# Kernel tuning notes

Measured on AMD Instinct MI355X. Metric: run time of the kernel, lower is better.

The kernel has to match this reference:

```python
import jax, jax.numpy as jnp
import numpy as np


def _layernorm(x, g, b, eps=1e-5):
    m = x.mean(-1, keepdims=True)
    v = ((x - m) ** 2).mean(-1, keepdims=True)
    return (x - m) * jax.lax.rsqrt(v + eps) * g + b


def _rmsnorm(x, w, eps=1e-6):
    return x * jax.lax.rsqrt((x * x).mean(-1, keepdims=True) + eps) * w


def setup_inputs() -> dict:
    key = jax.random.key(0)
    ks = jax.random.split(key, 8)
    B, T, S, C_img = 1, 3, 880, 3072
    C_mouse, D_hid, Dd = 2, 1024, 64
    vin = C_img + 12 * C_mouse  # 3096 = img_hidden + mouse_dim_in*vae_tcr*windows
    w = lambda k, shp: (jax.random.normal(k, shp, jnp.float32) * 0.02)
    return dict(
        x=jax.random.normal(ks[0], (B, T * S, C_img), jnp.float32),
        condition=jax.random.normal(ks[1], (B, 12, C_mouse), jnp.float32),
        w1=w(ks[2], (vin, D_hid)), b1=jnp.zeros((D_hid,), jnp.float32),
        w2=w(ks[3], (D_hid, D_hid)), b2=jnp.zeros((D_hid,), jnp.float32),
        ln_g=jnp.ones((D_hid,), jnp.float32), ln_b=jnp.zeros((D_hid,), jnp.float32),
        wqkv=w(ks[4], (D_hid, 3 * D_hid)), bqkv=jnp.zeros((3 * D_hid,), jnp.float32),
        qn_w=jnp.ones((Dd,), jnp.float32), kn_w=jnp.ones((Dd,), jnp.float32),
        wproj=w(ks[5], (D_hid, C_img)), bproj=jnp.zeros((C_img,), jnp.float32),
        H=22, W=40, temporal_shape=3, num_frame_per_block=3,
    )


def reference(x, condition, w1, b1, w2, b2, ln_g, ln_b, wqkv, bqkv,
              qn_w, kn_w, wproj, bproj, H, W, temporal_shape, num_frame_per_block):
    B, T_S, C_img = x.shape
    T = temporal_shape
    if condition.shape[1] > 9:
        condition = condition[:, -12:, :]
    _, N_frames, C = condition.shape
    action_len, pad_len = 20, 12
    pad = jnp.zeros((B, action_len - N_frames, C), condition.dtype)
    mouse_padded = jnp.concatenate([pad, condition], axis=1)  # [B, 20, C]
    # windowed gather: fixed small loop over num_frame_per_block (<=3)
    wins = jnp.stack([mouse_padded[:, i * 4:i * 4 + pad_len, :]
                      for i in range(num_frame_per_block)], axis=1)  # [B, F, 12, C]
    gm = wins.reshape(B, num_frame_per_block, pad_len * C)  # [B, F, 12C]
    S = 880  # hardcoded in original forward
    gm = jnp.broadcast_to(gm[:, None], (B, S, num_frame_per_block, pad_len * C))
    gm = gm.reshape(B * S, num_frame_per_block, pad_len * C)
    # fuse broadcast mouse features with image tokens (raw row-major reshape, as in torch)
    fused = jnp.concatenate([x.reshape(B * S, T, C_img), gm], axis=-1)  # [BS, T, C_img+12C]
    h = jax.nn.gelu(fused @ w1 + b1, approximate=True) @ w2 + b2
    h = _layernorm(h, ln_g, ln_b)  # [BS, T, D_hid]
    qkv = h @ wqkv + bqkv  # [BS, T, 3*D_hid]
    Dd = qn_w.shape[0]
    Hh = qkv.shape[-1] // (3 * Dd)
    qkv = qkv.reshape(B * S, T, 3, Hh, Dd)
    q, k, v = qkv[:, :, 0], qkv[:, :, 1], qkv[:, :, 2]
    q = _rmsnorm(q, qn_w).astype(v.dtype)
    k = _rmsnorm(k, kn_w).astype(v.dtype)
    # original flattens to one sequence of BS*T tokens for single_prefill (non-causal)
    N = B * S * T
    qf = q.reshape(N, Hh, Dd)
    kf = k.reshape(N, Hh, Dd)
    vf = v.reshape(N, Hh, Dd)
    scale = 1.0 / np.sqrt(Dd).astype(np.float32)
    scores = jnp.einsum('nhd,mhd->hnm', qf, kf) * scale  # [Hh, N, N]
    attn = jax.nn.softmax(scores, axis=-1)
    o = jnp.einsum('hnm,mhd->nhd', attn, vf)  # [N, Hh, Dd]
    # '(B S) T H D -> B (T S) (H D)'
    o = o.reshape(B, S, T, Hh, Dd).transpose(0, 2, 1, 3, 4).reshape(B, T * S, Hh * Dd)
    out = o @ wproj + bproj
    return x + out
```

## Files before the change

kernel.cpp:

```cpp
#include <hip/hip_runtime.h>
#include <hip/hip_bf16.h>

typedef __attribute__((ext_vector_type(8))) short short8;
typedef __attribute__((ext_vector_type(4))) short short4v;
typedef __attribute__((ext_vector_type(4))) unsigned uint4v;
typedef __attribute__((ext_vector_type(4))) float f32x4;
typedef __attribute__((ext_vector_type(16))) float f32x16;
typedef unsigned short u16;

#define ZERO16 (f32x16){0,0,0,0,0,0,0,0,0,0,0,0,0,0,0,0}

__device__ __forceinline__ float b2f(u16 h) {
    unsigned u = ((unsigned)h) << 16;
    float f; __builtin_memcpy(&f, &u, 4); return f;
}
__device__ __forceinline__ u16 f2b(float f) {
    __hip_bfloat16 h = __float2bfloat16(f);
    u16 r; __builtin_memcpy(&r, &h, 2); return r;
}
__device__ __forceinline__ void gload16(const void* g, void* l) {
    __builtin_amdgcn_global_load_lds(
        (const __attribute__((address_space(1))) unsigned*)g,
        (__attribute__((address_space(3))) unsigned*)l, 16, 0, 0);
}
__device__ __forceinline__ unsigned cvtpk_bf16(float lo, float hi) {
    unsigned d;
    asm("v_cvt_pk_bf16_f32 %0, %1, %2" : "=v"(d) : "v"(lo), "v"(hi));
    return d;
}

#define M_VALID 2640
#define M_PAD   2688
#define K1P     3072
#define DH      1024
#define CIMG    3072
#define NHEAD   16
#define NT      84
#define QTP     42
#define NSPLIT  3
#define TILES_PER_SPLIT 28
#define LOG2E   1.4426950408889634f

__global__ __launch_bounds__(256) void build_fused_kernel(
    const float* __restrict__ x, u16* __restrict__ fused)
{
    int n = blockIdx.x;
    int tid = threadIdx.x;
    const float* xr = x + (size_t)n * CIMG;
    u16* fr = fused + (size_t)n * K1P;
    for (int c = tid * 4; c < CIMG; c += 1024) {
        float4 v = *(const float4*)(xr + c);
        short4v w;
        w[0] = (short)f2b(v.x); w[1] = (short)f2b(v.y);
        w[2] = (short)f2b(v.z); w[3] = (short)f2b(v.w);
        *(short4v*)(fr + c) = w;
    }
}

__global__ __launch_bounds__(256) void bias1t_kernel(
    const float* __restrict__ w1, const float* __restrict__ b1,
    const float* __restrict__ cond, float* __restrict__ bias1t)
{
    int t = blockIdx.x;
    int col = blockIdx.y * 256 + threadIdx.x;
    float v = b1[col];
#pragma unroll
    for (int j = 0; j < 24; j++) {
        int f = t * 4 + (j >> 1);
        if (f >= 8) v += cond[(f - 8) * 2 + (j & 1)] * w1[(size_t)(3072 + j) * DH + col];
    }
    bias1t[t * DH + col] = v;
}

__global__ __launch_bounds__(256) void transpose_all_kernel(
    const float* __restrict__ w1, const float* __restrict__ w2,
    const float* __restrict__ wqkv, const float* __restrict__ wproj,
    u16* __restrict__ w1t, u16* __restrict__ w2t,
    u16* __restrict__ wqkvt, u16* __restrict__ wprojt)
{
    int b = blockIdx.x;
    const float* W; u16* Wt; int K, N, ldt, nx;
    if (b < 3072)      {            W = w1;    Wt = w1t;    K = 3072; N = DH;   ldt = 3072; nx = 32; }
    else if (b < 4096) { b -= 3072; W = w2;    Wt = w2t;    K = DH;   N = DH;   ldt = DH;   nx = 32; }
    else if (b < 7168) { b -= 4096; W = wqkv;  Wt = wqkvt;  K = DH;   N = 3072; ldt = DH;   nx = 96; }
    else               { b -= 7168; W = wproj; Wt = wprojt; K = DH;   N = CIMG; ldt = DH;   nx = 96; }
    __shared__ float t[32][33];
    int n0 = (b % nx) * 32, k0 = (b / nx) * 32;
    int x = threadIdx.x & 31, y0 = threadIdx.x >> 5;
    for (int yy = y0; yy < 32; yy += 8) {
        int k = k0 + yy, n = n0 + x;
        t[yy][x] = (k < K && n < N) ? W[(size_t)k * N + n] : 0.f;
    }
    __syncthreads();
    for (int yy = y0; yy < 32; yy += 8) {
        int n = n0 + yy, k = k0 + x;
        if (n < N && k < ldt) Wt[(size_t)n * ldt + k] = f2b(t[x][yy]);
    }
}

template<int EPI, int BM, int BN>
__global__ __launch_bounds__(256) void gemm_kernel(
    const u16* __restrict__ A, const u16* __restrict__ Bt,
    const float* __restrict__ bias, const float* __restrict__ resid,
    u16* __restrict__ Cb, float* __restrict__ Cf,
    int N, int K, int Mvalid)
{
    constexpr int MI  = BM / 32;
    constexpr int NJ  = BN / 32;
    constexpr int CA  = BM / 32;
    constexpr int CB  = BN / 32;
    constexpr unsigned ABYTES = BM * 128;
    constexpr unsigned BBYTES = BN * 128;
    constexpr unsigned STG = 2 * (ABYTES + BBYTES);
    constexpr unsigned CTW = BN + 4;
    constexpr unsigned CTB = BM * CTW * 4;
    constexpr int TPR = 256 / BM;
    __shared__ __align__(16) char smem[STG > CTB ? STG : CTB];

    const int tid = threadIdx.x;
    const int lane = tid & 63, wid = tid >> 6;
    const int l15 = lane & 15, l4 = lane >> 4;

    const int nx = N / BN;
    const int nwg = nx * (M_PAD / BM);
    const int bid = blockIdx.x;
    const int wgid = (bid & 7) * (nwg >> 3) + (bid >> 3);
    const int m0 = (wgid / nx) * BM, n0 = (wgid % nx) * BN;

    const int wr = (wid >> 1) * (BM / 2), wc = (wid & 1) * (BN / 2);

    const int srow = lane >> 3;
    const int scol = ((lane & 7) ^ (lane >> 3)) << 3;

    f32x4 acc[MI][NJ];
#pragma unroll
    for (int i = 0; i < MI; i++)
#pragma unroll
        for (int j = 0; j < NJ; j++) acc[i][j] = (f32x4){0.f, 0.f, 0.f, 0.f};

    const int nt = K >> 6;

    auto stage = [&](int buf, int k0) {
        char* Ab = smem + buf * ABYTES;
        char* Bb = smem + 2 * ABYTES + buf * BBYTES;
#pragma unroll
        for (int i = 0; i < CA; i++) {
            int c = wid * CA + i;
            gload16(A + (size_t)(m0 + c * 8 + srow) * K + k0 + scol,
                    Ab + c * 1024 + lane * 16);
        }
#pragma unroll
        for (int i = 0; i < CB; i++) {
            int c = wid * CB + i;
            gload16(Bt + (size_t)(n0 + c * 8 + srow) * K + k0 + scol,
                    Bb + c * 1024 + lane * 16);
        }
    };

    stage(0, 0);
    __syncthreads();
    int cur = 0;
    for (int t = 0; t < nt; t++) {
        if (t + 1 < nt) stage(cur ^ 1, (t + 1) * 64);
        const char* Ab = smem + cur * ABYTES;
        const char* Bb = smem + 2 * ABYTES + cur * BBYTES;
#pragma unroll
        for (int ki = 0; ki < 2; ki++) {
            short8 af[MI], bfr[NJ];
#pragma unroll
            for (int i = 0; i < MI; i++) {
                int row = wr + i * 16 + l15;
                af[i] = *(const short8*)(Ab + row * 128 + (((ki * 4 + l4) ^ (l15 & 7)) << 4));
            }
#pragma unroll
            for (int j = 0; j < NJ; j++) {
                int row = wc + j * 16 + l15;
                bfr[j] = *(const short8*)(Bb + row * 128 + (((ki * 4 + l4) ^ (l15 & 7)) << 4));
            }
            __builtin_amdgcn_s_setprio(1);
#pragma unroll
            for (int i = 0; i < MI; i++)
#pragma unroll
                for (int j = 0; j < NJ; j++)
                    acc[i][j] = __builtin_amdgcn_mfma_f32_16x16x32_bf16(af[i], bfr[j], acc[i][j], 0, 0, 0);
            __builtin_amdgcn_s_setprio(0);
        }
        __syncthreads();
        cur ^= 1;
    }

    float* Ct = (float*)smem;
#pragma unroll
    for (int i = 0; i < MI; i++)
#pragma unroll
        for (int j = 0; j < NJ; j++)
#pragma unroll
            for (int r = 0; r < 4; r++)
                Ct[(wr + i * 16 + l4 * 4 + r) * CTW + wc + j * 16 + l15] = acc[i][j][r];
    __syncthreads();

    const int row = tid / TPR;
    const int cb  = (tid % TPR) * (BN / TPR);
    const int grow = m0 + row;
    const int gcol = n0 + cb;
    if (EPI == 2) {
        if (grow < Mvalid) {
#pragma unroll
            for (int u = 0; u < BN / (4 * TPR); u++) {
                f32x4 v = *(const f32x4*)&Ct[row * CTW + cb + u * 4];
                float4 bv = *(const float4*)&bias[gcol + u * 4];
                float4 rv = *(const float4*)&resid[(size_t)grow * N + gcol + u * 4];
                float4 o;
                o.x = v[0] + bv.x + rv.x; o.y = v[1] + bv.y + rv.y;
                o.z = v[2] + bv.z + rv.z; o.w = v[3] + bv.w + rv.w;
                *(float4*)&Cf[(size_t)grow * N + gcol + u * 4] = o;
            }
        }
    } else {
        const float* bb = bias + (EPI == 0 ? (size_t)(grow % 3) * N : 0);
        u16 tmp[BN / TPR];
#pragma unroll
        for (int u = 0; u < BN / (4 * TPR); u++) {
            f32x4 v = *(const f32x4*)&Ct[row * CTW + cb + u * 4];
            float4 bv = *(const float4*)&bb[gcol + u * 4];
#pragma unroll
            for (int e = 0; e < 4; e++) {
                float val = v[e] + ((const float*)&bv)[e];
                if (EPI == 0) {
                    float tt = val + 0.044715f * val * val * val;
                    val = 0.5f * val * (1.0f + tanhf(0.7978845608028654f * tt));
                }
                tmp[u * 4 + e] = f2b(val);
            }
        }
#pragma unroll
        for (int u = 0; u < BN / (8 * TPR); u++)
            *(short8*)(Cb + (size_t)grow * N + gcol + u * 8) = *(const short8*)&tmp[u * 8];
    }
}

__global__ __launch_bounds__(256) void ln_kernel(
    const u16* __restrict__ h2, const float* __restrict__ g,
    const float* __restrict__ b, u16* __restrict__ out)
{
    int row = blockIdx.x;
    int tid = threadIdx.x;
    const u16* p = h2 + (size_t)row * DH;
    float v[4];
#pragma unroll
    for (int i = 0; i < 4; i++) v[i] = b2f(p[tid * 4 + i]);
    float s1 = v[0] + v[1] + v[2] + v[3];
    float s2 = v[0]*v[0] + v[1]*v[1] + v[2]*v[2] + v[3]*v[3];
    for (int m = 1; m < 64; m <<= 1) { s1 += __shfl_xor(s1, m); s2 += __shfl_xor(s2, m); }
    __shared__ float a1[4], a2[4];
    int w = tid >> 6;
    if ((tid & 63) == 0) { a1[w] = s1; a2[w] = s2; }
    __syncthreads();
    s1 = a1[0] + a1[1] + a1[2] + a1[3];
    s2 = a2[0] + a2[1] + a2[2] + a2[3];
    float mean = s1 * (1.0f / 1024.0f);
    float var = s2 * (1.0f / 1024.0f) - mean * mean;
    float rs = rsqrtf(var + 1e-5f);
    u16* q = out + (size_t)row * DH;
#pragma unroll
    for (int i = 0; i < 4; i++) {
        int c = tid * 4 + i;
        q[c] = f2b((v[i] - mean) * rs * g[c] + b[c]);
    }
}

__global__ __launch_bounds__(256) void fragmentize_kernel(
    const u16* __restrict__ qkv, const float* __restrict__ qw, const float* __restrict__ kw,
    u16* __restrict__ Qf, u16* __restrict__ Kf, u16* __restrict__ Vf)
{
    __shared__ u16 Vlds[8 * 32 * 80];
    const int kt = blockIdx.x;
    const int hg = blockIdx.y;
    const int tid = threadIdx.x;
    const int t32 = tid >> 3, c8 = tid & 7;
    const int n = kt * 32 + t32;
    const u16* row = qkv + (size_t)n * 3072;

#pragma unroll
    for (int hh = 0; hh < 8; hh++) {
        short8 v = *(const short8*)(row + 2048 + (hg * 8 + hh) * 64 + c8 * 8);
        *(short8*)(&Vlds[(hh * 32 + t32) * 80 + c8 * 8]) = v;
    }

    float sq[8], sk[8];
#pragma unroll
    for (int hh = 0; hh < 8; hh++) {
        int h = hg * 8 + hh;
        short8 qv = *(const short8*)(row + h * 64 + c8 * 8);
        short8 kv = *(const short8*)(row + 1024 + h * 64 + c8 * 8);
        float aq = 0.f, ak = 0.f;
#pragma unroll
        for (int e = 0; e < 8; e++) {
            float fq = b2f((u16)qv[e]); aq += fq * fq;
            float fk = b2f((u16)kv[e]); ak += fk * fk;
        }
        sq[hh] = aq; sk[hh] = ak;
    }
#pragma unroll
    for (int m = 1; m < 8; m <<= 1) {
#pragma unroll
        for (int hh = 0; hh < 8; hh++) {
            sq[hh] += __shfl_xor(sq[hh], m);
            sk[hh] += __shfl_xor(sk[hh], m);
        }
    }

    float qwv[8], kwv[8];
#pragma unroll
    for (int e = 0; e < 8; e++) { qwv[e] = qw[c8 * 8 + e]; kwv[e] = kw[c8 * 8 + e]; }

#pragma unroll
    for (int hh = 0; hh < 8; hh++) {
        int h = hg * 8 + hh;
        float rq = rsqrtf(sq[hh] * (1.0f / 64.0f) + 1e-6f) * (0.125f * LOG2E);
        float rk = rsqrtf(sk[hh] * (1.0f / 64.0f) + 1e-6f);
        short8 qv = *(const short8*)(row + h * 64 + c8 * 8);
        short8 kv = *(const short8*)(row + 1024 + h * 64 + c8 * 8);
        short8 qo, ko;
#pragma unroll
        for (int e = 0; e < 8; e++) {
            qo[e] = (short)f2b(b2f((u16)qv[e]) * rq * qwv[e]);
            ko[e] = (short)f2b(b2f((u16)kv[e]) * rk * kwv[e]);
        }
        size_t base = (((size_t)(h * NT + kt) * 4 + (c8 >> 1)) << 9) + t32 * 16 + (c8 & 1) * 8;
        *(short8*)(Qf + base) = qo;
        *(short8*)(Kf + base) = ko;
    }

    __syncthreads();

    const int fd = tid >> 6;
    const int lkq = (tid & 63) >> 1, lhi = tid & 1;
#pragma unroll
    for (int hh = 0; hh < 8; hh++) {
        int h = hg * 8 + hh;
        short8 o;
#pragma unroll
        for (int e = 0; e < 8; e++)
            o[e] = (short)Vlds[(hh * 32 + (fd & 1) * 16 + lhi * 8 + e) * 80 + (fd >> 1) * 32 + lkq];
        *(short8*)(Vf + (((size_t)(h * NT + kt) * 4 + fd) << 9) + lkq * 16 + lhi * 8) = o;
    }
}

__device__ __forceinline__ void attn_tile(
    f32x16& st, float& lr, f32x16& o0, f32x16& o1,
    const u16* __restrict__ Vh, int tile, int lxy)
{
    short8 vv[4];
#pragma unroll
    for (int fd = 0; fd < 4; fd++)
        vv[fd] = *(const short8*)(Vh + (((size_t)tile * 4 + fd) << 9) + lxy);

    float p[16];
#pragma unroll
    for (int r = 0; r < 16; r++) p[r] = __builtin_amdgcn_exp2f(st[r]);
    float s0 = (p[0] + p[1]) + (p[2] + p[3]);
    float s1 = (p[4] + p[5]) + (p[6] + p[7]);
    float s2 = (p[8] + p[9]) + (p[10] + p[11]);
    float s3 = (p[12] + p[13]) + (p[14] + p[15]);
    float sum = (s0 + s1) + (s2 + s3);
    lr += sum + __shfl_xor(sum, 32);

    unsigned a0 = cvtpk_bf16(p[0], p[1]),   a1 = cvtpk_bf16(p[2], p[3]);
    unsigned a2 = cvtpk_bf16(p[4], p[5]),   a3 = cvtpk_bf16(p[6], p[7]);
    unsigned a4 = cvtpk_bf16(p[8], p[9]),   a5 = cvtpk_bf16(p[10], p[11]);
    unsigned a6 = cvtpk_bf16(p[12], p[13]), a7 = cvtpk_bf16(p[14], p[15]);
    asm("v_permlane32_swap_b32 %0, %1" : "+v"(a0), "+v"(a2));
    asm("v_permlane32_swap_b32 %0, %1" : "+v"(a1), "+v"(a3));
    asm("v_permlane32_swap_b32 %0, %1" : "+v"(a4), "+v"(a6));
    asm("v_permlane32_swap_b32 %0, %1" : "+v"(a5), "+v"(a7));
    uint4v u0 = {a0, a1, a2, a3}, u1 = {a4, a5, a6, a7};
    short8 pa0, pa1;
    __builtin_memcpy(&pa0, &u0, 16);
    __builtin_memcpy(&pa1, &u1, 16);

    __builtin_amdgcn_s_setprio(1);
    o0 = __builtin_amdgcn_mfma_f32_32x32x16_bf16(pa0, vv[0], o0, 0, 0, 0);
    o0 = __builtin_amdgcn_mfma_f32_32x32x16_bf16(pa1, vv[1], o0, 0, 0, 0);
    o1 = __builtin_amdgcn_mfma_f32_32x32x16_bf16(pa0, vv[2], o1, 0, 0, 0);
    o1 = __builtin_amdgcn_mfma_f32_32x32x16_bf16(pa1, vv[3], o1, 0, 0, 0);
    __builtin_amdgcn_s_setprio(0);
}

__global__ __launch_bounds__(128, 2) void attn_kernel(
    const u16* __restrict__ Qf, const u16* __restrict__ Kf,
    const u16* __restrict__ Vf, u16* __restrict__ part, float* __restrict__ ml)
{
    const int nwg = NSPLIT * NHEAD * QTP;
    const int bid = blockIdx.x;
    const int wgid = (bid & 7) * (nwg >> 3) + (bid >> 3);
    const int s   = wgid / (NHEAD * QTP);
    const int rem = wgid % (NHEAD * QTP);
    const int h   = rem / QTP;
    const int qtp = rem % QTP;
    const int wid = threadIdx.x >> 6;
    const int qt  = qtp * 2 + wid;
    const int lane = threadIdx.x & 63;
    const int kq = lane & 31;
    const int hi = lane >> 5;
    const int q0 = qt * 32;
    const int lxy = kq * 16 + hi * 8;
    const u16* Kh = Kf + ((size_t)h * NT * 4 << 9);
    const u16* Vh = Vf + ((size_t)h * NT * 4 << 9);

    short8 qf[4];
#pragma unroll
    for (int d = 0; d < 4; d++)
        qf[d] = *(const short8*)(Qf + (((size_t)(h * NT + qt) * 4 + d) << 9) + lxy);

    f32x16 o0 = ZERO16, o1 = ZERO16;
    float lr = 0.f;
    const int ts0 = s * TILES_PER_SPLIT;

    auto loadK = [&](short8* k, int tile) {
#pragma unroll
        for (int d = 0; d < 4; d++)
            k[d] = *(const short8*)(Kh + (((size_t)tile * 4 + d) << 9) + lxy);
    };
    auto qk = [&](const short8* k) {
        f32x16 st = ZERO16;
        __builtin_amdgcn_s_setprio(1);
#pragma unroll
        for (int d = 0; d < 4; d++)
            st = __builtin_amdgcn_mfma_f32_32x32x16_bf16(k[d], qf[d], st, 0, 0, 0);
        __builtin_amdgcn_s_setprio(0);
        return st;
    };
    auto mask = [&](f32x16& st, int tile) {
        const int k0 = tile * 32;
        if (k0 + 32 > M_VALID) {
#pragma unroll
            for (int r = 0; r < 16; r++) {
                int key = k0 + (r & 3) + 8 * (r >> 2) + 4 * hi;
                if (key >= M_VALID) st[r] = -3.0e38f;
            }
        }
    };

    short8 kfA[4], kfB[4];
    loadK(kfA, ts0);
    loadK(kfB, ts0 + 1);

    for (int i = 0; i < TILES_PER_SPLIT; i += 2) {
        const int t0 = ts0 + i, t1 = t0 + 1;
        f32x16 st0 = qk(kfA);
        f32x16 st1 = qk(kfB);
        if (i + 2 < TILES_PER_SPLIT) { loadK(kfA, t0 + 2); loadK(kfB, t0 + 3); }
        mask(st0, t0);
        attn_tile(st0, lr, o0, o1, Vh, t0, lxy);
        mask(st1, t1);
        attn_tile(st1, lr, o0, o1, Vh, t1, lxy);
    }

#pragma unroll
    for (int r = 0; r < 16; r++) {
        int rl = (r & 3) + 8 * (r >> 2) + 4 * hi;
        int qrow = q0 + rl;
        if (qrow < M_VALID) {
            u16* pp = part + ((size_t)s * M_PAD + qrow) * DH + h * 64;
            pp[kq] = f2b(o0[r]);
            pp[kq + 32] = f2b(o1[r]);
        }
    }
    if (hi == 0 && q0 + kq < M_VALID)
        ml[((size_t)s * NHEAD + h) * M_PAD + q0 + kq] = lr;
}

__global__ __launch_bounds__(256) void attn_merge_kernel(
    const u16* __restrict__ part, const float* __restrict__ ml, u16* __restrict__ obf)
{
    const int q = blockIdx.x;
    const int t = threadIdx.x;
    const int h = t >> 4, i = t & 15;
    float L = 0.f;
#pragma unroll
    for (int s = 0; s < NSPLIT; s++)
        L += ml[((size_t)s * NHEAD + h) * M_PAD + q];
    float inv = 1.0f / L;
    float4 acc = {0.f, 0.f, 0.f, 0.f};
#pragma unroll
    for (int s = 0; s < NSPLIT; s++) {
        short4v v = *(const short4v*)(part + ((size_t)s * M_PAD + q) * DH + h * 64 + i * 4);
        acc.x += b2f((u16)v[0]); acc.y += b2f((u16)v[1]);
        acc.z += b2f((u16)v[2]); acc.w += b2f((u16)v[3]);
    }
    int mrow = (q % 3) * 880 + q / 3;
    short4v w;
    w[0] = (short)f2b(acc.x * inv); w[1] = (short)f2b(acc.y * inv);
    w[2] = (short)f2b(acc.z * inv); w[3] = (short)f2b(acc.w * inv);
    *(short4v*)(obf + (size_t)mrow * DH + h * 64 + i * 4) = w;
}

extern "C" void kernel_launch(void* const* d_in, const int* in_sizes, int n_in,
                              void* d_out, int out_size, void* d_ws, size_t ws_size,
                              hipStream_t stream)
{
    const float* x      = (const float*)d_in[0];
    const float* cond   = (const float*)d_in[1];
    const float* w1     = (const float*)d_in[2];
    const float* b1     = (const float*)d_in[3];
    const float* w2     = (const float*)d_in[4];
    const float* b2     = (const float*)d_in[5];
    const float* ln_g   = (const float*)d_in[6];
    const float* ln_b   = (const float*)d_in[7];
    const float* wqkv   = (const float*)d_in[8];
    const float* bqkv   = (const float*)d_in[9];
    const float* qn_w   = (const float*)d_in[10];
    const float* kn_w   = (const float*)d_in[11];
    const float* wproj  = (const float*)d_in[12];
    const float* bproj  = (const float*)d_in[13];
    float* out = (float*)d_out;

    char* ws = (char*)d_ws;
    size_t off = 0;
    auto alloc = [&](size_t bytes) { size_t o = off; off += (bytes + 255) & ~(size_t)255; return o; };

    size_t off_fused  = alloc((size_t)M_PAD * K1P * 2);
    size_t off_w1t    = alloc((size_t)DH * K1P * 2);
    size_t off_w2t    = alloc((size_t)DH * DH * 2);
    size_t off_wqkvt  = alloc((size_t)3072 * DH * 2);
    size_t off_wprojt = alloc((size_t)CIMG * DH * 2);
    size_t off_h1     = alloc((size_t)M_PAD * DH * 2);
    size_t off_h2     = alloc((size_t)M_PAD * DH * 2);
    size_t off_h2ln   = alloc((size_t)M_PAD * DH * 2);
    size_t off_qkv    = alloc((size_t)M_PAD * 3072 * 2);
    size_t off_qf     = alloc((size_t)NHEAD * NT * 4 * 512 * 2);
    size_t off_kf     = alloc((size_t)NHEAD * NT * 4 * 512 * 2);
    size_t off_vf     = alloc((size_t)NHEAD * NT * 4 * 512 * 2);
    size_t off_obf    = alloc((size_t)M_PAD * DH * 2);
    size_t off_b1t    = alloc((size_t)3 * DH * 4);
    (void)ws_size;

    u16* fused  = (u16*)(ws + off_fused);
    u16* w1t    = (u16*)(ws + off_w1t);
    u16* w2t    = (u16*)(ws + off_w2t);
    u16* wqkvt  = (u16*)(ws + off_wqkvt);
    u16* wprojt = (u16*)(ws + off_wprojt);
    u16* h1     = (u16*)(ws + off_h1);
    u16* h2     = (u16*)(ws + off_h2);
    u16* h2ln   = (u16*)(ws + off_h2ln);
    u16* qkvb   = (u16*)(ws + off_qkv);
    u16* Qf     = (u16*)(ws + off_qf);
    u16* Kf     = (u16*)(ws + off_kf);
    u16* Vf     = (u16*)(ws + off_vf);
    u16* obf    = (u16*)(ws + off_obf);
    float* b1t  = (float*)(ws + off_b1t);
    u16* part   = (u16*)(ws + off_h1);
    float* mlbf = (float*)(ws + off_fused);

    build_fused_kernel<<<M_VALID, 256, 0, stream>>>(x, fused);
    bias1t_kernel<<<dim3(3, 4), 256, 0, stream>>>(w1, b1, cond, b1t);
    transpose_all_kernel<<<10240, 256, 0, stream>>>(w1, w2, wqkv, wproj, w1t, w2t, wqkvt, wprojt);

    gemm_kernel<0, 64, 64><<<dim3((DH / 64) * (M_PAD / 64)), 256, 0, stream>>>(fused, w1t, b1t, nullptr, h1, nullptr, DH, K1P, M_PAD);
    gemm_kernel<1, 64, 64><<<dim3((DH / 64) * (M_PAD / 64)), 256, 0, stream>>>(h1, w2t, b2, nullptr, h2, nullptr, DH, DH, M_PAD);
    ln_kernel<<<M_PAD, 256, 0, stream>>>(h2, ln_g, ln_b, h2ln);
    gemm_kernel<1, 128, 128><<<dim3((3072 / 128) * (M_PAD / 128)), 256, 0, stream>>>(h2ln, wqkvt, bqkv, nullptr, qkvb, nullptr, 3072, DH, M_PAD);
    fragmentize_kernel<<<dim3(NT, 2), 256, 0, stream>>>(qkvb, qn_w, kn_w, Qf, Kf, Vf);
    attn_kernel<<<dim3(NSPLIT * NHEAD * QTP), 128, 0, stream>>>(Qf, Kf, Vf, part, mlbf);
    attn_merge_kernel<<<M_VALID, 256, 0, stream>>>(part, mlbf, obf);
    gemm_kernel<2, 128, 128><<<dim3((CIMG / 128) * (M_PAD / 128)), 256, 0, stream>>>(obf, wprojt, bproj, x, nullptr, out, CIMG, DH, M_VALID);
}
```

Measured before the change: 192.0 us.

## Use 4-wave attention workgroups with single-tile K prefetch and early V loads

The attention kernel now launches 256-thread workgroups (4 waves, each owning a query tile) with launch bounds raised to 4 blocks per CU, halving the number of workgroups. The two-tile K double-buffered loop is replaced by a single-tile loop that issues V loads at the start of each iteration and prefetches only the next K tile. This cuts register pressure so more waves fit per CU, letting hardware interleaving hide memory latency instead of explicit software pipelining. The risk is less instruction-level parallelism per wave, and the serial softmax sum adds a dependency chain.

Result: no change. 188.3 us (-1.9%).

```diff
diff --git a/kernel.cpp b/kernel.cpp
--- a/kernel.cpp
+++ b/kernel.cpp
@@ -36,7 +36,7 @@
 #define CIMG    3072
 #define NHEAD   16
 #define NT      84
-#define QTP     42
+#define QG      21
 #define NSPLIT  3
 #define TILES_PER_SPLIT 28
 #define LOG2E   1.4426950408889634f
@@ -348,22 +348,12 @@
 }
 
 __device__ __forceinline__ void attn_tile(
-    f32x16& st, float& lr, f32x16& o0, f32x16& o1,
-    const u16* __restrict__ Vh, int tile, int lxy)
-{
-    short8 vv[4];
-#pragma unroll
-    for (int fd = 0; fd < 4; fd++)
-        vv[fd] = *(const short8*)(Vh + (((size_t)tile * 4 + fd) << 9) + lxy);
-
+    f32x16& st, float& lr, f32x16& o0, f32x16& o1, const short8* vv)
+{
+    float sum = 0.f;
     float p[16];
 #pragma unroll
-    for (int r = 0; r < 16; r++) p[r] = __builtin_amdgcn_exp2f(st[r]);
-    float s0 = (p[0] + p[1]) + (p[2] + p[3]);
-    float s1 = (p[4] + p[5]) + (p[6] + p[7]);
-    float s2 = (p[8] + p[9]) + (p[10] + p[11]);
-    float s3 = (p[12] + p[13]) + (p[14] + p[15]);
-    float sum = (s0 + s1) + (s2 + s3);
+    for (int r = 0; r < 16; r++) { p[r] = __builtin_amdgcn_exp2f(st[r]); sum += p[r]; }
     lr += sum + __shfl_xor(sum, 32);
 
     unsigned a0 = cvtpk_bf16(p[0], p[1]),   a1 = cvtpk_bf16(p[2], p[3]);
@@ -387,19 +377,19 @@
     __builtin_amdgcn_s_setprio(0);
 }
 
-__global__ __launch_bounds__(128, 2) void attn_kernel(
+__global__ __launch_bounds__(256, 4) void attn_kernel(
     const u16* __restrict__ Qf, const u16* __restrict__ Kf,
     const u16* __restrict__ Vf, u16* __restrict__ part, float* __restrict__ ml)
 {
-    const int nwg = NSPLIT * NHEAD * QTP;
+    const int nwg = NSPLIT * NHEAD * QG;
     const int bid = blockIdx.x;
     const int wgid = (bid & 7) * (nwg >> 3) + (bid >> 3);
-    const int s   = wgid / (NHEAD * QTP);
-    const int rem = wgid % (NHEAD * QTP);
-    const int h   = rem / QTP;
-    const int qtp = rem % QTP;
+    const int s   = wgid / (NHEAD * QG);
+    const int rem = wgid % (NHEAD * QG);
+    const int h   = rem / QG;
+    const int qg  = rem % QG;
     const int wid = threadIdx.x >> 6;
-    const int qt  = qtp * 2 + wid;
+    const int qt  = qg * 4 + wid;
     const int lane = threadIdx.x & 63;
     const int kq = lane & 31;
     const int hi = lane >> 5;
@@ -415,24 +405,34 @@
 
     f32x16 o0 = ZERO16, o1 = ZERO16;
     float lr = 0.f;
+
     const int ts0 = s * TILES_PER_SPLIT;
-
-    auto loadK = [&](short8* k, int tile) {
-#pragma unroll
-        for (int d = 0; d < 4; d++)
-            k[d] = *(const short8*)(Kh + (((size_t)tile * 4 + d) << 9) + lxy);
-    };
-    auto qk = [&](const short8* k) {
+    short8 kf[4];
+#pragma unroll
+    for (int d = 0; d < 4; d++)
+        kf[d] = *(const short8*)(Kh + (((size_t)ts0 * 4 + d) << 9) + lxy);
+
+    for (int i = 0; i < TILES_PER_SPLIT; i++) {
+        const int tile = ts0 + i;
+        const int k0 = tile * 32;
+        short8 vv[4];
+#pragma unroll
+        for (int fd = 0; fd < 4; fd++)
+            vv[fd] = *(const short8*)(Vh + (((size_t)tile * 4 + fd) << 9) + lxy);
+
         f32x16 st = ZERO16;
         __builtin_amdgcn_s_setprio(1);
 #pragma unroll
         for (int d = 0; d < 4; d++)
-            st = __builtin_amdgcn_mfma_f32_32x32x16_bf16(k[d], qf[d], st, 0, 0, 0);
+            st = __builtin_amdgcn_mfma_f32_32x32x16_bf16(kf[d], qf[d], st, 0, 0, 0);
         __builtin_amdgcn_s_setprio(0);
-        return st;
-    };
-    auto mask = [&](f32x16& st, int tile) {
-        const int k0 = tile * 32;
+
+        if (i < TILES_PER_SPLIT - 1) {
+#pragma unroll
+            for (int d = 0; d < 4; d++)
+                kf[d] = *(const short8*)(Kh + (((size_t)(tile + 1) * 4 + d) << 9) + lxy);
+        }
+
         if (k0 + 32 > M_VALID) {
 #pragma unroll
             for (int r = 0; r < 16; r++) {
@@ -440,21 +440,7 @@
                 if (key >= M_VALID) st[r] = -3.0e38f;
             }
         }
-    };
-
-    short8 kfA[4], kfB[4];
-    loadK(kfA, ts0);
-    loadK(kfB, ts0 + 1);
-
-    for (int i = 0; i < TILES_PER_SPLIT; i += 2) {
-        const int t0 = ts0 + i, t1 = t0 + 1;
-        f32x16 st0 = qk(kfA);
-        f32x16 st1 = qk(kfB);
-        if (i + 2 < TILES_PER_SPLIT) { loadK(kfA, t0 + 2); loadK(kfB, t0 + 3); }
-        mask(st0, t0);
-        attn_tile(st0, lr, o0, o1, Vh, t0, lxy);
-        mask(st1, t1);
-        attn_tile(st1, lr, o0, o1, Vh, t1, lxy);
+        attn_tile(st, lr, o0, o1, vv);
     }
 
 #pragma unroll
@@ -562,7 +548,7 @@
     ln_kernel<<<M_PAD, 256, 0, stream>>>(h2, ln_g, ln_b, h2ln);
     gemm_kernel<1, 128, 128><<<dim3((3072 / 128) * (M_PAD / 128)), 256, 0, stream>>>(h2ln, wqkvt, bqkv, nullptr, qkvb, nullptr, 3072, DH, M_PAD);
     fragmentize_kernel<<<dim3(NT, 2), 256, 0, stream>>>(qkvb, qn_w, kn_w, Qf, Kf, Vf);
-    attn_kernel<<<dim3(NSPLIT * NHEAD * QTP), 128, 0, stream>>>(Qf, Kf, Vf, part, mlbf);
+    attn_kernel<<<dim3(NSPLIT * NHEAD * QG), 256, 0, stream>>>(Qf, Kf, Vf, part, mlbf);
     attn_merge_kernel<<<M_VALID, 256, 0, stream>>>(part, mlbf, obf);
     gemm_kernel<2, 128, 128><<<dim3((CIMG / 128) * (M_PAD / 128)), 256, 0, stream>>>(obf, wprojt, bproj, x, nullptr, out, CIMG, DH, M_VALID);
 }
```
